# Optimization experiments

Hardware: AMD Instinct MI355X
Metric: run time of the kernel (lower is better)

The kernel has to match this reference:

```python
import jax, jax.numpy as jnp
import numpy as np

D_INNER, D_STATE, DT_RANK = 2048, 16, 128
BATCH, SEQ = 2, 2048


def setup_inputs() -> dict:
    key = jax.random.key(0)
    ks = jax.random.split(key, 6)
    x = jax.random.normal(ks[0], (BATCH, SEQ, D_INNER), dtype=jnp.float32)
    # A_log initialized uniform(-4, -1) per _init_parameters
    A_log = jax.random.uniform(ks[1], (D_INNER, D_STATE), minval=-4.0, maxval=-1.0, dtype=jnp.float32)
    D = jnp.ones((D_INNER,), dtype=jnp.float32)
    # torch Linear weights: [out_features, in_features], kaiming-uniform-ish scale
    x_proj_w = jax.random.normal(ks[2], (DT_RANK + 2 * D_STATE, D_INNER), dtype=jnp.float32) / np.sqrt(D_INNER)
    dt_proj_w = jax.random.normal(ks[3], (D_INNER, DT_RANK), dtype=jnp.float32) / np.sqrt(DT_RANK)
    dt_std = DT_RANK ** (-0.5)
    dt_proj_b = jax.random.uniform(ks[4], (D_INNER,), minval=-dt_std, maxval=dt_std, dtype=jnp.float32)
    return {"x": x, "A_log": A_log, "D": D, "x_proj_w": x_proj_w,
            "dt_proj_w": dt_proj_w, "dt_proj_b": dt_proj_b}


def _selective_scan(u, delta, A, B, C, D):
    # u, delta: [b, l, d]; A: [d, n]; B, C: [b, l, n]; D: [d]
    dA = jnp.exp(delta[..., None] * A[None, None])          # [b, l, d, n]
    dBu = (delta * u)[..., None] * B[:, :, None, :]         # [b, l, d, n]

    def step(h, inp):
        dA_t, dBu_t, C_t = inp                              # [b,d,n],[b,d,n],[b,n]
        h = dA_t * h + dBu_t
        y_t = jnp.einsum('bdn,bn->bd', h, C_t)
        return h, y_t

    h0 = jnp.zeros((u.shape[0], u.shape[2], A.shape[1]), dtype=u.dtype)
    xs = (jnp.moveaxis(dA, 1, 0), jnp.moveaxis(dBu, 1, 0), jnp.moveaxis(C, 1, 0))
    _, ys = jax.lax.scan(step, h0, xs)                      # ys: [l, b, d]
    y = jnp.moveaxis(ys, 0, 1)
    return y + u * D[None, None, :]


def reference(x, A_log, D, x_proj_w, dt_proj_w, dt_proj_b):
    # x: [b, l, d_inner]
    x_dbl = jnp.einsum('bld,ed->ble', x, x_proj_w)          # [b, l, dt_rank + 2n]
    delta_r = x_dbl[..., :DT_RANK]
    B = x_dbl[..., DT_RANK:DT_RANK + D_STATE]
    C = x_dbl[..., DT_RANK + D_STATE:]
    delta = jnp.einsum('blr,dr->bld', delta_r, dt_proj_w) + dt_proj_b
    delta = jax.nn.softplus(delta)                          # delta_softplus=True
    A = -jnp.exp(A_log)
    return _selective_scan(x, delta, A, B, C, D)
```

## Files before the change

### kernel.cpp

```cpp
#include <hip/hip_runtime.h>
#include <hip/hip_bf16.h>
#include <math.h>

#define DI   2048
#define DS   16
#define DTR  128
#define NBATCH 2
#define SEQ  2048
#define ROWS (NBATCH*SEQ)
#define NE   (DTR + 2*DS)
#define NC   64
#define LC   (SEQ/NC)

typedef float f32x4 __attribute__((ext_vector_type(4)));
typedef short s16x8 __attribute__((ext_vector_type(8)));
typedef short s16x4 __attribute__((ext_vector_type(4)));

__device__ inline short f2bf(float f) {
    unsigned u = __builtin_bit_cast(unsigned, f);
    u += 0x7FFFu + ((u >> 16) & 1u);
    return (short)(u >> 16);
}

__device__ inline unsigned pk2(float lo, float hi) {
    union { __hip_bfloat162 h; unsigned u; } cv;
    cv.h = __float22bfloat162_rn(float2{lo, hi});
    return cv.u;
}
__device__ inline unsigned packdu(short dbf, float xf) {
    return ((unsigned)(unsigned short)f2bf(xf) << 16) | (unsigned)(unsigned short)dbf;
}

__global__ __launch_bounds__(256) void k_castw(const float* __restrict__ w,
                                               const float* __restrict__ dtw,
                                               short* __restrict__ wb,
                                               short* __restrict__ dtwb) {
    int i = blockIdx.x*256 + threadIdx.x;
    if (i < 81920) {
        float4 v = ((const float4*)w)[i];
        s16x4 o = { f2bf(v.x), f2bf(v.y), f2bf(v.z), f2bf(v.w) };
        *(s16x4*)(wb + 4*i) = o;
    } else if (i < 147456) {
        int j = i - 81920;
        float4 v = ((const float4*)dtw)[j];
        s16x4 o = { f2bf(v.x), f2bf(v.y), f2bf(v.z), f2bf(v.w) };
        *(s16x4*)(dtwb + 4*j) = o;
    }
}

__global__ __launch_bounds__(256) void k_gemm1(const float* __restrict__ x,
                                               const short* __restrict__ wb,
                                               short* __restrict__ dRb,
                                               float* __restrict__ Bm,
                                               float* __restrict__ Cm) {
    const int wave = blockIdx.x*4 + (threadIdx.x >> 6);
    const int lane = threadIdx.x & 63;
    const int m16  = wave & 255;
    const int half = wave >> 8;
    const int r = lane & 15, g = lane >> 4;
    f32x4 acc[5];
    #pragma unroll
    for (int i = 0; i < 5; i++) acc[i] = (f32x4){0.f,0.f,0.f,0.f};

    const float* xp = x + (size_t)(m16*16 + r)*DI + g*8;
    const short* wbase = wb + (size_t)(half*80 + r)*DI + g*8;
    #pragma unroll 2
    for (int kk = 0; kk < 64; ++kk) {
        const int k0 = kk*32;
        float4 xa = *(const float4*)(xp + k0);
        float4 xc = *(const float4*)(xp + k0 + 4);
        union { s16x8 v; unsigned u[4]; } af;
        af.u[0] = pk2(xa.x, xa.y);
        af.u[1] = pk2(xa.z, xa.w);
        af.u[2] = pk2(xc.x, xc.y);
        af.u[3] = pk2(xc.z, xc.w);
        #pragma unroll
        for (int nf = 0; nf < 5; ++nf) {
            s16x8 bfrag = *(const s16x8*)(wbase + (size_t)nf*16*DI + k0);
            acc[nf] = __builtin_amdgcn_mfma_f32_16x16x32_bf16(af.v, bfrag, acc[nf], 0, 0, 0);
        }
    }
    const int orow = m16*16 + g*4;
    #pragma unroll
    for (int nf = 0; nf < 5; ++nf) {
        const int gnf = half*5 + nf;
        const int col = gnf*16 + r;
        #pragma unroll
        for (int j = 0; j < 4; ++j) {
            const int row = orow + j;
            float v = acc[nf][j];
            if (gnf < 8)       dRb[(size_t)row*DTR + col]        = f2bf(v);
            else if (gnf == 8) Bm [(size_t)row*DS + (col - 128)] = v;
            else               Cm [(size_t)row*DS + (col - 144)] = v;
        }
    }
}

__global__ __launch_bounds__(256) void k_gemm2(const short* __restrict__ dRb,
                                               const short* __restrict__ dtwb,
                                               const float* __restrict__ bias,
                                               unsigned short* __restrict__ deltab) {
    const int wave = blockIdx.x*4 + (threadIdx.x >> 6);
    const int lane = threadIdx.x & 63;
    const int m16 = wave >> 5, nt = wave & 31;
    const int r = lane & 15, g = lane >> 4;

    s16x8 a[4];
    const short* ap = dRb + (size_t)(m16*16 + r)*DTR + g*8;
    #pragma unroll
    for (int ks = 0; ks < 4; ++ks) a[ks] = *(const s16x8*)(ap + ks*32);

    f32x4 acc[4];
    #pragma unroll
    for (int i = 0; i < 4; i++) acc[i] = (f32x4){0.f,0.f,0.f,0.f};

    #pragma unroll
    for (int nf = 0; nf < 4; ++nf) {
        const short* bp = dtwb + (size_t)(nt*64 + nf*16 + r)*DTR + g*8;
        #pragma unroll
        for (int ks = 0; ks < 4; ++ks) {
            s16x8 b = *(const s16x8*)(bp + ks*32);
            acc[nf] = __builtin_amdgcn_mfma_f32_16x16x32_bf16(a[ks], b, acc[nf], 0, 0, 0);
        }
    }
    const int orow = m16*16 + g*4;
    #pragma unroll
    for (int nf = 0; nf < 4; ++nf) {
        const int col = nt*64 + nf*16 + r;
        const float bb = bias[col];
        #pragma unroll
        for (int j = 0; j < 4; ++j) {
            float v = acc[nf][j] + bb;
            float sp = fmaxf(v, 0.f) + __logf(1.f + __expf(-fabsf(v)));
            deltab[(size_t)(orow + j)*DI + col] = (unsigned short)f2bf(sp);
        }
    }
}

__global__ __launch_bounds__(256) void k_scan1(const unsigned short* __restrict__ deltab,
                                               const float* __restrict__ x,
                                               const float* __restrict__ Bm,
                                               const float* __restrict__ A_log,
                                               float* __restrict__ aprod,
                                               float* __restrict__ rsum) {
    __shared__ unsigned lxd[LC][64];
    __shared__ float lB[LC][DS];
    const int tid = threadIdx.x;
    const int bb = blockIdx.x & 31;
    const int b  = (blockIdx.x >> 5) & 1;
    const int c  = blockIdx.x >> 6;
    const int d0 = bb*64;
    const int lbase = c*LC;

    {
        const unsigned short* dsrc = deltab + ((size_t)(b*SEQ + lbase))*DI + d0;
        const float*          xsrc = x      + ((size_t)(b*SEQ + lbase))*DI + d0;
        const int row = tid >> 4, col = (tid & 15)*4;
        #pragma unroll
        for (int i = 0; i < 2; i++) {
            s16x4  dv = *(const s16x4*) (dsrc + (size_t)(row + 16*i)*DI + col);
            float4 xv = *(const float4*)(xsrc + (size_t)(row + 16*i)*DI + col);
            uint4 o;
            o.x = packdu(dv[0], xv.x);
            o.y = packdu(dv[1], xv.y);
            o.z = packdu(dv[2], xv.z);
            o.w = packdu(dv[3], xv.w);
            *(uint4*)&lxd[row + 16*i][col] = o;
        }
        if (tid < 128) {
            const float* bsrc = Bm + ((size_t)(b*SEQ + lbase))*DS;
            *(float4*)&lB[tid >> 2][(tid & 3)*4] = *(const float4*)(bsrc + tid*4);
        }
    }

    const int lane = tid & 63, widx = tid >> 6;
    const int dlow = lane & 15, q = lane >> 4;
    const int dcol = widx*16 + dlow;
    const int d = d0 + dcol;
    const int n0 = 4*q;

    float4 Alg = *(const float4*)(A_log + (size_t)d*DS + n0);
    float An[4] = { -__expf(Alg.x), -__expf(Alg.y), -__expf(Alg.z), -__expf(Alg.w) };
    float r[4] = {0.f,0.f,0.f,0.f};
    float S = 0.f;

    __syncthreads();

    #pragma unroll 8
    for (int tt = 0; tt < LC; ++tt) {
        unsigned v = lxd[tt][dcol];
        float dlt = __builtin_bit_cast(float, v << 16);
        float u   = __builtin_bit_cast(float, v & 0xffff0000u);
        float du  = dlt * u;
        S += dlt;
        float4 bv = *(const float4*)&lB[tt][n0];
        float bbv[4] = {bv.x, bv.y, bv.z, bv.w};
        #pragma unroll
        for (int j = 0; j < 4; ++j) {
            float da = __expf(dlt * An[j]);
            r[j] = fmaf(da, r[j], du * bbv[j]);
        }
    }
    size_t base = (((size_t)c*NBATCH + b)*DI + d)*DS + n0;
    *(float4*)(aprod + base) = (float4){ __expf(An[0]*S), __expf(An[1]*S),
                                         __expf(An[2]*S), __expf(An[3]*S) };
    *(float4*)(rsum  + base) = (float4){ r[0], r[1], r[2], r[3] };
}

__global__ __launch_bounds__(256) void k_mid(float* ah,
                                             const float* __restrict__ rsum) {
    int gid = blockIdx.x*256 + threadIdx.x;
    int n = gid & 15;
    int d = (gid >> 4) & (DI-1);
    int b = gid >> 15;
    float h = 0.f;
    for (int c = 0; c < NC; c++) {
        size_t idx = (((size_t)c*NBATCH + b)*DI + d)*DS + n;
        float a  = ah[idx];
        float rr = rsum[idx];
        ah[idx] = h;
        h = fmaf(a, h, rr);
    }
}

__global__ __launch_bounds__(256) void k_scan2(const unsigned short* __restrict__ deltab,
                                               const float* __restrict__ x,
                                               const float* __restrict__ Bm,
                                               const float* __restrict__ Cm,
                                               const float* __restrict__ A_log,
                                               const float* __restrict__ Dv,
                                               const float* __restrict__ hin,
                                               float* __restrict__ y) {
    __shared__ unsigned lxd[LC][64];
    __shared__ float lB[LC][DS];
    __shared__ float lC[LC][DS];
    const int tid = threadIdx.x;
    const int bb = blockIdx.x & 31;
    const int b  = (blockIdx.x >> 5) & 1;
    const int c  = blockIdx.x >> 6;
    const int d0 = bb*64;
    const int lbase = c*LC;

    {
        const unsigned short* dsrc = deltab + ((size_t)(b*SEQ + lbase))*DI + d0;
        const float*          xsrc = x      + ((size_t)(b*SEQ + lbase))*DI + d0;
        const int row = tid >> 4, col = (tid & 15)*4;
        #pragma unroll
        for (int i = 0; i < 2; i++) {
            s16x4  dv = *(const s16x4*) (dsrc + (size_t)(row + 16*i)*DI + col);
            float4 xv = *(const float4*)(xsrc + (size_t)(row + 16*i)*DI + col);
            uint4 o;
            o.x = packdu(dv[0], xv.x);
            o.y = packdu(dv[1], xv.y);
            o.z = packdu(dv[2], xv.z);
            o.w = packdu(dv[3], xv.w);
            *(uint4*)&lxd[row + 16*i][col] = o;
        }
        if (tid < 128) {
            const float* bsrc = Bm + ((size_t)(b*SEQ + lbase))*DS;
            const float* csrc = Cm + ((size_t)(b*SEQ + lbase))*DS;
            *(float4*)&lB[tid >> 2][(tid & 3)*4] = *(const float4*)(bsrc + tid*4);
            *(float4*)&lC[tid >> 2][(tid & 3)*4] = *(const float4*)(csrc + tid*4);
        }
    }

    const int lane = tid & 63, widx = tid >> 6;
    const int dlow = lane & 15, q = lane >> 4;
    const int dcol = widx*16 + dlow;
    const int d = d0 + dcol;
    const int n0 = 4*q;

    float4 Alg = *(const float4*)(A_log + (size_t)d*DS + n0);
    float An[4] = { -__expf(Alg.x), -__expf(Alg.y), -__expf(Alg.z), -__expf(Alg.w) };
    size_t base = (((size_t)c*NBATCH + b)*DI + d)*DS + n0;
    float4 hv = *(const float4*)(hin + base);
    float h[4] = {hv.x, hv.y, hv.z, hv.w};
    const float Dd = Dv[d];
    float* yp = y + ((size_t)(b*SEQ + lbase))*DI + d;

    __syncthreads();

    #pragma unroll 8
    for (int tt = 0; tt < LC; ++tt) {
        unsigned v = lxd[tt][dcol];
        float dlt = __builtin_bit_cast(float, v << 16);
        float u   = __builtin_bit_cast(float, v & 0xffff0000u);
        float du  = dlt * u;
        float4 bv = *(const float4*)&lB[tt][n0];
        float4 cv = *(const float4*)&lC[tt][n0];
        float bbv[4] = {bv.x, bv.y, bv.z, bv.w};
        float ccv[4] = {cv.x, cv.y, cv.z, cv.w};
        float acc = 0.f;
        #pragma unroll
        for (int j = 0; j < 4; ++j) {
            float da = __expf(dlt * An[j]);
            h[j] = fmaf(da, h[j], du * bbv[j]);
            acc  = fmaf(h[j], ccv[j], acc);
        }
        acc += __shfl_xor(acc, 16);
        acc += __shfl_xor(acc, 32);
        if (q == 0) yp[(size_t)tt*DI] = fmaf(u, Dd, acc);
    }
}

extern "C" void kernel_launch(void* const* d_in, const int* in_sizes, int n_in,
                              void* d_out, int out_size, void* d_ws, size_t ws_size,
                              hipStream_t stream) {
    const float* x     = (const float*)d_in[0];
    const float* A_log = (const float*)d_in[1];
    const float* Dv    = (const float*)d_in[2];
    const float* xpw   = (const float*)d_in[3];
    const float* dtw   = (const float*)d_in[4];
    const float* dtb   = (const float*)d_in[5];
    float* out = (float*)d_out;

    const size_t SCN = (size_t)NC*NBATCH*DS*DI;

    float* ws    = (float*)d_ws;
    unsigned short* deltab = (unsigned short*)ws;
    float* aprod = ws + ((size_t)ROWS*DI/2);
    float* rsum  = aprod + SCN;
    float* Bm    = rsum + SCN;
    float* Cm    = Bm + (size_t)ROWS*DS;
    short* dRb   = (short*)(Cm + (size_t)ROWS*DS);
    short* wb    = dRb + (size_t)ROWS*DTR;
    short* dtwb  = wb  + (size_t)160*2048;

    k_castw<<<576, 256, 0, stream>>>(xpw, dtw, wb, dtwb);
    k_gemm1<<<128, 256, 0, stream>>>(x, wb, dRb, Bm, Cm);
    k_gemm2<<<2048, 256, 0, stream>>>(dRb, dtwb, dtb, deltab);
    k_scan1<<<4096, 256, 0, stream>>>(deltab, x, Bm, A_log, aprod, rsum);
    k_mid<<<256, 256, 0, stream>>>(aprod, rsum);
    k_scan2<<<4096, 256, 0, stream>>>(deltab, x, Bm, Cm, A_log, Dv, aprod, out);
}
```

Before: 228.5 us.

## Split-K gemm1 across waves and drop LDS staging in scan kernels

gemm1 now launches 256 blocks of 8 waves, each pair of waves splitting K four ways and reducing partial MFMA accumulators through shared memory, so more of the GPU is occupied than with the former 128 blocks. The scan kernels drop the shared-memory staging of delta/x/B/C and the block barrier, and instead have each wave read directly from global memory per timestep. Exp is rewritten as exp2 with a pre-scaled A. This removes the cast of x to bf16 inside the scan (x is now read in fp32), which also changes the numerics slightly. The cost is strided, uncoalesced-ish per-step global loads in place of bulk tile loads into LDS.

```diff
diff --git a/kernel.cpp b/kernel.cpp
--- a/kernel.cpp
+++ b/kernel.cpp
@@ -16,6 +16,8 @@
 typedef short s16x8 __attribute__((ext_vector_type(8)));
 typedef short s16x4 __attribute__((ext_vector_type(4)));
 
+#define L2E 1.4426950408889634f
+
 __device__ inline short f2bf(float f) {
     unsigned u = __builtin_bit_cast(unsigned, f);
     u += 0x7FFFu + ((u >> 16) & 1u);
@@ -26,9 +28,6 @@
     union { __hip_bfloat162 h; unsigned u; } cv;
     cv.h = __float22bfloat162_rn(float2{lo, hi});
     return cv.u;
-}
-__device__ inline unsigned packdu(short dbf, float xf) {
-    return ((unsigned)(unsigned short)f2bf(xf) << 16) | (unsigned)(unsigned short)dbf;
 }
 
 __global__ __launch_bounds__(256) void k_castw(const float* __restrict__ w,
@@ -48,24 +47,24 @@
     }
 }
 
-__global__ __launch_bounds__(256) void k_gemm1(const float* __restrict__ x,
+__global__ __launch_bounds__(512) void k_gemm1(const float* __restrict__ x,
                                                const short* __restrict__ wb,
                                                short* __restrict__ dRb,
                                                float* __restrict__ Bm,
                                                float* __restrict__ Cm) {
-    const int wave = blockIdx.x*4 + (threadIdx.x >> 6);
-    const int lane = threadIdx.x & 63;
-    const int m16  = wave & 255;
-    const int half = wave >> 8;
+    __shared__ float lred[2][3][5][64][4];
+    const int tid  = threadIdx.x;
+    const int w    = tid >> 6;
+    const int lane = tid & 63;
+    const int half = w & 1, kq = w >> 1;
+    const int m16  = blockIdx.x;
     const int r = lane & 15, g = lane >> 4;
-    f32x4 acc[5];
-    #pragma unroll
-    for (int i = 0; i < 5; i++) acc[i] = (f32x4){0.f,0.f,0.f,0.f};
-
-    const float* xp = x + (size_t)(m16*16 + r)*DI + g*8;
-    const short* wbase = wb + (size_t)(half*80 + r)*DI + g*8;
-    #pragma unroll 2
-    for (int kk = 0; kk < 64; ++kk) {
+
+    f32x4 acc[5] = {};
+    const float* xp    = x  + (size_t)(m16*16 + r)*DI + g*8 + kq*512;
+    const short* wbase = wb + (size_t)(half*80 + r)*DI + g*8 + kq*512;
+    #pragma unroll 4
+    for (int kk = 0; kk < 16; ++kk) {
         const int k0 = kk*32;
         float4 xa = *(const float4*)(xp + k0);
         float4 xc = *(const float4*)(xp + k0 + 4);
@@ -80,18 +79,31 @@
             acc[nf] = __builtin_amdgcn_mfma_f32_16x16x32_bf16(af.v, bfrag, acc[nf], 0, 0, 0);
         }
     }
-    const int orow = m16*16 + g*4;
-    #pragma unroll
-    for (int nf = 0; nf < 5; ++nf) {
-        const int gnf = half*5 + nf;
-        const int col = gnf*16 + r;
-        #pragma unroll
-        for (int j = 0; j < 4; ++j) {
-            const int row = orow + j;
-            float v = acc[nf][j];
-            if (gnf < 8)       dRb[(size_t)row*DTR + col]        = f2bf(v);
-            else if (gnf == 8) Bm [(size_t)row*DS + (col - 128)] = v;
-            else               Cm [(size_t)row*DS + (col - 144)] = v;
+    if (kq > 0) {
+        #pragma unroll
+        for (int nf = 0; nf < 5; ++nf)
+            *(f32x4*)&lred[half][kq-1][nf][lane][0] = acc[nf];
+    }
+    __syncthreads();
+    if (kq == 0) {
+        #pragma unroll
+        for (int nf = 0; nf < 5; ++nf)
+            #pragma unroll
+            for (int p = 0; p < 3; ++p)
+                acc[nf] += *(const f32x4*)&lred[half][p][nf][lane][0];
+        const int orow = m16*16 + g*4;
+        #pragma unroll
+        for (int nf = 0; nf < 5; ++nf) {
+            const int gnf = half*5 + nf;
+            const int col = gnf*16 + r;
+            #pragma unroll
+            for (int j = 0; j < 4; ++j) {
+                const int row = orow + j;
+                float v = acc[nf][j];
+                if (gnf < 8)       dRb[(size_t)row*DTR + col]        = f2bf(v);
+                else if (gnf == 8) Bm [(size_t)row*DS + (col - 128)] = v;
+                else               Cm [(size_t)row*DS + (col - 144)] = v;
+            }
         }
     }
 }
@@ -110,10 +122,7 @@
     #pragma unroll
     for (int ks = 0; ks < 4; ++ks) a[ks] = *(const s16x8*)(ap + ks*32);
 
-    f32x4 acc[4];
-    #pragma unroll
-    for (int i = 0; i < 4; i++) acc[i] = (f32x4){0.f,0.f,0.f,0.f};
-
+    f32x4 acc[4] = {};
     #pragma unroll
     for (int nf = 0; nf < 4; ++nf) {
         const short* bp = dtwb + (size_t)(nt*64 + nf*16 + r)*DTR + g*8;
@@ -143,68 +152,45 @@
                                                const float* __restrict__ A_log,
                                                float* __restrict__ aprod,
                                                float* __restrict__ rsum) {
-    __shared__ unsigned lxd[LC][64];
-    __shared__ float lB[LC][DS];
-    const int tid = threadIdx.x;
-    const int bb = blockIdx.x & 31;
-    const int b  = (blockIdx.x >> 5) & 1;
-    const int c  = blockIdx.x >> 6;
-    const int d0 = bb*64;
-    const int lbase = c*LC;
-
-    {
-        const unsigned short* dsrc = deltab + ((size_t)(b*SEQ + lbase))*DI + d0;
-        const float*          xsrc = x      + ((size_t)(b*SEQ + lbase))*DI + d0;
-        const int row = tid >> 4, col = (tid & 15)*4;
-        #pragma unroll
-        for (int i = 0; i < 2; i++) {
-            s16x4  dv = *(const s16x4*) (dsrc + (size_t)(row + 16*i)*DI + col);
-            float4 xv = *(const float4*)(xsrc + (size_t)(row + 16*i)*DI + col);
-            uint4 o;
-            o.x = packdu(dv[0], xv.x);
-            o.y = packdu(dv[1], xv.y);
-            o.z = packdu(dv[2], xv.z);
-            o.w = packdu(dv[3], xv.w);
-            *(uint4*)&lxd[row + 16*i][col] = o;
-        }
-        if (tid < 128) {
-            const float* bsrc = Bm + ((size_t)(b*SEQ + lbase))*DS;
-            *(float4*)&lB[tid >> 2][(tid & 3)*4] = *(const float4*)(bsrc + tid*4);
-        }
-    }
-
-    const int lane = tid & 63, widx = tid >> 6;
+    const int tid  = threadIdx.x;
+    const int lane = tid & 63;
+    const int w    = blockIdx.x*4 + (tid >> 6);
     const int dlow = lane & 15, q = lane >> 4;
-    const int dcol = widx*16 + dlow;
-    const int d = d0 + dcol;
+    const int d16  = w & 127;
+    const int rest = w >> 7;
+    const int b = rest & 1, c = rest >> 1;
+    const int d = d16*16 + dlow;
     const int n0 = 4*q;
 
     float4 Alg = *(const float4*)(A_log + (size_t)d*DS + n0);
-    float An[4] = { -__expf(Alg.x), -__expf(Alg.y), -__expf(Alg.z), -__expf(Alg.w) };
+    float An2[4] = { -__expf(Alg.x)*L2E, -__expf(Alg.y)*L2E,
+                     -__expf(Alg.z)*L2E, -__expf(Alg.w)*L2E };
     float r[4] = {0.f,0.f,0.f,0.f};
     float S = 0.f;
 
-    __syncthreads();
-
-    #pragma unroll 8
+    const unsigned short* dp = deltab + (size_t)b*SEQ*DI + d;
+    const float* xp = x  + (size_t)b*SEQ*DI + d;
+    const float* bp = Bm + (size_t)b*SEQ*DS + n0;
+    const int lbase = c*LC;
+    #pragma unroll 4
     for (int tt = 0; tt < LC; ++tt) {
-        unsigned v = lxd[tt][dcol];
-        float dlt = __builtin_bit_cast(float, v << 16);
-        float u   = __builtin_bit_cast(float, v & 0xffff0000u);
+        const int l = lbase + tt;
+        float dlt = __builtin_bit_cast(float, (unsigned)dp[(size_t)l*DI] << 16);
+        float u   = xp[(size_t)l*DI];
         float du  = dlt * u;
         S += dlt;
-        float4 bv = *(const float4*)&lB[tt][n0];
+        float4 bv = *(const float4*)(bp + (size_t)l*DS);
         float bbv[4] = {bv.x, bv.y, bv.z, bv.w};
         #pragma unroll
         for (int j = 0; j < 4; ++j) {
-            float da = __expf(dlt * An[j]);
+            float da = exp2f(An2[j] * dlt);
             r[j] = fmaf(da, r[j], du * bbv[j]);
         }
     }
     size_t base = (((size_t)c*NBATCH + b)*DI + d)*DS + n0;
-    *(float4*)(aprod + base) = (float4){ __expf(An[0]*S), __expf(An[1]*S),
-                                         __expf(An[2]*S), __expf(An[3]*S) };
-    *(float4*)(rsum  + base) = (float4){ r[0], r[1], r[2], r[3] };
+    *(f32x4*)(aprod + base) = (f32x4){ exp2f(An2[0]*S), exp2f(An2[1]*S),
+                                       exp2f(An2[2]*S), exp2f(An2[3]*S) };
+    *(f32x4*)(rsum  + base) = (f32x4){ r[0], r[1], r[2], r[3] };
 }
 
 __global__ __launch_bounds__(256) void k_mid(float* ah,
@@ -231,75 +217,50 @@
                                                const float* __restrict__ Dv,
                                                const float* __restrict__ hin,
                                                float* __restrict__ y) {
-    __shared__ unsigned lxd[LC][64];
-    __shared__ float lB[LC][DS];
-    __shared__ float lC[LC][DS];
-    const int tid = threadIdx.x;
-    const int bb = blockIdx.x & 31;
-    const int b  = (blockIdx.x >> 5) & 1;
-    const int c  = blockIdx.x >> 6;
-    const int d0 = bb*64;
-    const int lbase = c*LC;
-
-    {
-        const unsigned short* dsrc = deltab + ((size_t)(b*SEQ + lbase))*DI + d0;
-        const float*          xsrc = x      + ((size_t)(b*SEQ + lbase))*DI + d0;
-        const int row = tid >> 4, col = (tid & 15)*4;
-        #pragma unroll
-        for (int i = 0; i < 2; i++) {
-            s16x4  dv = *(const s16x4*) (dsrc + (size_t)(row + 16*i)*DI + col);
-            float4 xv = *(const float4*)(xsrc + (size_t)(row + 16*i)*DI + col);
-            uint4 o;
-            o.x = packdu(dv[0], xv.x);
-            o.y = packdu(dv[1], xv.y);
-            o.z = packdu(dv[2], xv.z);
-            o.w = packdu(dv[3], xv.w);
-            *(uint4*)&lxd[row + 16*i][col] = o;
-        }
-        if (tid < 128) {
-            const float* bsrc = Bm + ((size_t)(b*SEQ + lbase))*DS;
-            const float* csrc = Cm + ((size_t)(b*SEQ + lbase))*DS;
-            *(float4*)&lB[tid >> 2][(tid & 3)*4] = *(const float4*)(bsrc + tid*4);
-            *(float4*)&lC[tid >> 2][(tid & 3)*4] = *(const float4*)(csrc + tid*4);
-        }
-    }
-
-    const int lane = tid & 63, widx = tid >> 6;
+    const int tid  = threadIdx.x;
+    const int lane = tid & 63;
+    const int w    = blockIdx.x*4 + (tid >> 6);
     const int dlow = lane & 15, q = lane >> 4;
-    const int dcol = widx*16 + dlow;
-    const int d = d0 + dcol;
+    const int d16  = w & 127;
+    const int rest = w >> 7;
+    const int b = rest & 1, c = rest >> 1;
+    const int d = d16*16 + dlow;
     const int n0 = 4*q;
 
     float4 Alg = *(const float4*)(A_log + (size_t)d*DS + n0);
-    float An[4] = { -__expf(Alg.x), -__expf(Alg.y), -__expf(Alg.z), -__expf(Alg.w) };
+    float An2[4] = { -__expf(Alg.x)*L2E, -__expf(Alg.y)*L2E,
+                     -__expf(Alg.z)*L2E, -__expf(Alg.w)*L2E };
     size_t base = (((size_t)c*NBATCH + b)*DI + d)*DS + n0;
     float4 hv = *(const float4*)(hin + base);
     float h[4] = {hv.x, hv.y, hv.z, hv.w};
     const float Dd = Dv[d];
-    float* yp = y + ((size_t)(b*SEQ + lbase))*DI + d;
-
-    __syncthreads();
-
-    #pragma unroll 8
+
+    const unsigned short* dp = deltab + (size_t)b*SEQ*DI + d;
+    const float* xp = x  + (size_t)b*SEQ*DI + d;
+    const float* bp = Bm + (size_t)b*SEQ*DS + n0;
+    const float* cp = Cm + (size_t)b*SEQ*DS + n0;
+    float* yp = y + (size_t)b*SEQ*DI + d;
+    const int lbase = c*LC;
+    #pragma unroll 4
     for (int tt = 0; tt < LC; ++tt) {
-        unsigned v = lxd[tt][dcol];
-        float dlt = __builtin_bit_cast(float, v << 16);
-        float u   = __builtin_bit_cast(float, v & 0xffff0000u);
+        const int l = lbase + tt;
+        float dlt = __builtin_bit_cast(float, (unsigned)dp[(size_t)l*DI] << 16);
+        float u   = xp[(size_t)l*DI];
         float du  = dlt * u;
-        float4 bv = *(const float4*)&lB[tt][n0];
-        float4 cv = *(const float4*)&lC[tt][n0];
+        float4 bv = *(const float4*)(bp + (size_t)l*DS);
+        float4 cv = *(const float4*)(cp + (size_t)l*DS);
         float bbv[4] = {bv.x, bv.y, bv.z, bv.w};
         float ccv[4] = {cv.x, cv.y, cv.z, cv.w};
         float acc = 0.f;
         #pragma unroll
         for (int j = 0; j < 4; ++j) {
-            float da = __expf(dlt * An[j]);
+            float da = exp2f(An2[j] * dlt);
             h[j] = fmaf(da, h[j], du * bbv[j]);
             acc  = fmaf(h[j], ccv[j], acc);
         }
         acc += __shfl_xor(acc, 16);
         acc += __shfl_xor(acc, 32);
-        if (q == 0) yp[(size_t)tt*DI] = fmaf(u, Dd, acc);
+        if (q == 0) yp[(size_t)l*DI] = fmaf(u, Dd, acc);
     }
 }
 
@@ -327,7 +288,7 @@
     short* dtwb  = wb  + (size_t)160*2048;
 
     k_castw<<<576, 256, 0, stream>>>(xpw, dtw, wb, dtwb);
-    k_gemm1<<<128, 256, 0, stream>>>(x, wb, dRb, Bm, Cm);
+    k_gemm1<<<256, 512, 0, stream>>>(x, wb, dRb, Bm, Cm);
     k_gemm2<<<2048, 256, 0, stream>>>(dRb, dtwb, dtb, deltab);
     k_scan1<<<4096, 256, 0, stream>>>(deltab, x, Bm, A_log, aprod, rsum);
     k_mid<<<256, 256, 0, stream>>>(aprod, rsum);
```

Result: slower. 234.2 us (+2.5%).
